# Kernel optimization log

Measured on AMD Instinct MI355X. Metric: run time of the kernel, lower is better.

The kernel has to match this reference:

```python
import jax, jax.numpy as jnp
import numpy as np

N = 100000
E = 3200000
D = 128
EPS = 1e-5


def setup_inputs() -> dict:
    key = jax.random.key(0)
    ks = jax.random.split(key, 9)
    h = jax.random.normal(ks[0], (N, D), dtype=jnp.float32)
    src = jax.random.randint(ks[1], (E,), 0, N, dtype=jnp.int64)
    dst = jax.random.randint(ks[2], (E,), 0, N, dtype=jnp.int64)
    s = 1.0 / np.sqrt(D)
    W_self = jax.random.uniform(ks[3], (D, D), jnp.float32, -s, s)
    W_neigh = jax.random.uniform(ks[4], (D, D), jnp.float32, -s, s)
    b = jax.random.uniform(ks[5], (D,), jnp.float32, -s, s)
    gamma = jnp.ones((D,), jnp.float32)
    beta = jnp.zeros((D,), jnp.float32)
    return {"h": h, "src": src, "dst": dst, "W_self": W_self,
            "W_neigh": W_neigh, "b": b, "gamma": gamma, "beta": beta}


def reference(h, src, dst, W_self, W_neigh, b, gamma, beta):
    # --- SAGEConv, mean aggregator (dropout p=0 -> identity) ---
    # gather source features along edges, segment-mean into destination nodes
    neigh_sum = jax.ops.segment_sum(h[src], dst, num_segments=N)      # [N, D]
    deg = jax.ops.segment_sum(jnp.ones((E,), h.dtype), dst, num_segments=N)
    neigh = neigh_sum / jnp.maximum(deg, 1.0)[:, None]                # [N, D]
    rst = h @ W_self + neigh @ W_neigh + b                            # [N, D]
    rst = jax.nn.relu(rst)                                            # activation
    # --- BatchNorm1d (training-mode batch statistics) ---
    mean = jnp.mean(rst, axis=0)
    var = jnp.var(rst, axis=0)
    rst = (rst - mean) * jax.lax.rsqrt(var + EPS) * gamma + beta
    # --- residual (in_feats == out_feats) ---
    return h + rst
```

## Files before the change

kernel.cpp:

```cpp
#include <hip/hip_runtime.h>

#define DCAP 2432
#define NBMAX 1600
#define SCATB 256
#define SORTCAP 12544
#define CONVB 2048
#define WPB 128
#define ZB 7
#define GB 1024
#define EORDCAP 3456

typedef __attribute__((ext_vector_type(2))) float f32x2;
typedef __attribute__((ext_vector_type(4))) float f32x4;
typedef __attribute__((ext_vector_type(8))) short bf16x8;

__device__ __forceinline__ unsigned short f2bf(float f) {
  union { float f; unsigned u; } c; c.f = f;
  unsigned u = c.u;
  unsigned r = u + 0x7FFFu + ((u >> 16) & 1u);
  return (unsigned short)(r >> 16);
}
__device__ __forceinline__ float bf2f(unsigned short s) {
  union { unsigned u; float f; } c; c.u = ((unsigned)s) << 16;
  return c.f;
}

__global__ __launch_bounds__(256) void k_pre(const float* __restrict__ h,
                                             unsigned short* __restrict__ X,
                                             unsigned* __restrict__ X8,
                                             const float* __restrict__ Ws,
                                             const float* __restrict__ Wn,
                                             unsigned short* __restrict__ Wt,
                                             int* __restrict__ gcur,
                                             int nnodes, int NB) {
  int t = threadIdx.x;
  int bid = blockIdx.x;
  if (bid < CONVB) {
    int stride = CONVB * 256;
    int total = nnodes * 32;
    for (int i = bid * 256 + t; i < total; i += stride) {
      int n = i >> 5, c = i & 31;
      float4 v = *(const float4*)(h + (long)n * 128 + c * 4);
      ushort4 o;
      o.x = f2bf(v.x); o.y = f2bf(v.y); o.z = f2bf(v.z); o.w = f2bf(v.w);
      *(ushort4*)(X + (long)n * 256 + c * 4) = o;
      int p8 = __builtin_amdgcn_cvt_pk_fp8_f32(v.x, v.y, 0, false);
      p8 = __builtin_amdgcn_cvt_pk_fp8_f32(v.z, v.w, p8, true);
      X8[(long)n * 32 + c] = (unsigned)p8;
    }
  } else if (bid < CONVB + WPB) {
    int i = (bid - CONVB) * 256 + t;
    int col = i >> 8, k = i & 255;
    float v = (k < 128) ? Ws[k * 128 + col] : Wn[(k - 128) * 128 + col];
    Wt[col * 256 + k] = f2bf(v);
  } else {
    int i = (bid - CONVB - WPB) * 256 + t;
    if (i < NB) gcur[i] = 0;
    if (i < 32) X8[(long)nnodes * 32 + i] = 0u;
  }
}

__global__ __launch_bounds__(1024) void k_scat(const int* __restrict__ dst,
                                               const int* __restrict__ src,
                                               unsigned* __restrict__ esort,
                                               int* __restrict__ gcur,
                                               int E, int NB, int chunk) {
  __shared__ int cnt[NBMAX];
  __shared__ int lstart[NBMAX];
  __shared__ int gbase[NBMAX];
  __shared__ int tsum[1024];
  __shared__ unsigned sorted[SORTCAP];
  __shared__ unsigned short sbk[SORTCAP];
  int t = threadIdx.x, bid = blockIdx.x;
  int e0 = bid * chunk;
  int e1 = e0 + chunk; if (e1 > E) e1 = E;
  int n = e1 - e0;
  for (int i = t; i < NB; i += 1024) cnt[i] = 0;
  __syncthreads();
  for (int i = t; i < n; i += 1024)
    atomicAdd(&cnt[dst[e0 + i] >> 6], 1);
  __syncthreads();
  int b0 = 2 * t, b1 = 2 * t + 1;
  int c0 = (b0 < NB) ? cnt[b0] : 0;
  int c1 = (b1 < NB) ? cnt[b1] : 0;
  tsum[t] = c0 + c1;
  __syncthreads();
  for (int off = 1; off < 1024; off <<= 1) {
    int v = (t >= off) ? tsum[t - off] : 0;
    __syncthreads();
    tsum[t] += v;
    __syncthreads();
  }
  int ex = tsum[t] - (c0 + c1);
  if (b0 < NB) {
    lstart[b0] = ex;
    cnt[b0] = ex;
    if (b1 < NB) { lstart[b1] = ex + c0; cnt[b1] = ex + c0; }
  }
  __syncthreads();
  for (int i = t; i < n; i += 1024) {
    int d = dst[e0 + i];
    int bb = d >> 6;
    int p = atomicAdd(&cnt[bb], 1);
    sorted[p] = ((unsigned)src[e0 + i] << 6) | (unsigned)(d & 63);
    sbk[p] = (unsigned short)bb;
  }
  __syncthreads();
  for (int bb = t; bb < NB; bb += 1024) {
    int len = cnt[bb] - lstart[bb];
    gbase[bb] = len ? atomicAdd(&gcur[bb], len) : 0;
  }
  __syncthreads();
  for (int i = t; i < n; i += 1024) {
    int bb = sbk[i];
    int pos = gbase[bb] + (i - lstart[bb]);
    if (pos < DCAP)
      esort[(long)bb * DCAP + pos] = sorted[i];
  }
}

__global__ __launch_bounds__(256) void k_aggb(unsigned short* __restrict__ X,
                                              const unsigned char* __restrict__ X8,
                                              const unsigned* __restrict__ esort,
                                              const int* __restrict__ gcur,
                                              int nnodes) {
  __shared__ unsigned eord[EORDCAP];
  __shared__ int dcnt[64], dstart[64], dcur[64], sc[64];
  int t = threadIdx.x;
  int b = blockIdx.x;
  int cntE = gcur[b]; if (cntE > DCAP) cntE = DCAP;
  const unsigned* ep = esort + (long)b * DCAP;
  if (t < 64) dcnt[t] = 0;
  __syncthreads();
  for (int i = t; i < cntE; i += 256)
    atomicAdd(&dcnt[ep[i] & 63u], 1);
  __syncthreads();
  int plen_t = 0;
  if (t < 64) { plen_t = (dcnt[t] + 15) & ~15; sc[t] = plen_t; }
  __syncthreads();
  for (int off = 1; off < 64; off <<= 1) {
    int v = (t < 64 && t >= off) ? sc[t - off] : 0;
    __syncthreads();
    if (t < 64) sc[t] += v;
    __syncthreads();
  }
  if (t < 64) { int ex = sc[t] - plen_t; dstart[t] = ex; dcur[t] = ex; }
  __syncthreads();
  int tot = sc[63];
  for (int i = t; i < tot; i += 256) eord[i] = (unsigned)nnodes;
  __syncthreads();
  for (int i = t; i < cntE; i += 256) {
    unsigned e = ep[i];
    int pos = atomicAdd(&dcur[e & 63u], 1);
    eord[pos] = e >> 6;
  }
  __syncthreads();

  int lane = t & 63, w = t >> 6;
  int qt = lane >> 4, ql = lane & 15;
  int ndst = nnodes - b * 64; if (ndst > 64) ndst = 64;
  for (int dl = w; dl < ndst; dl += 4) {
    int start = dstart[dl], dn = dcnt[dl];
    int plen = (dn + 15) & ~15;
    f32x2 acc[2][4];
#pragma unroll
    for (int u = 0; u < 2; u++)
#pragma unroll
      for (int j = 0; j < 4; j++) { acc[u][j].x = 0.f; acc[u][j].y = 0.f; }
    int i = 0;
    for (; i + 32 <= plen; i += 32) {
      uint2 v[8];
#pragma unroll
      for (int u = 0; u < 8; u++) {
        unsigned e = eord[start + i + u * 4 + qt];
        v[u] = *(const uint2*)(X8 + e * 128u + ql * 8u);
      }
#pragma unroll
      for (int u = 0; u < 8; u++) {
        acc[u & 1][0] += __builtin_amdgcn_cvt_pk_f32_fp8(v[u].x, false);
        acc[u & 1][1] += __builtin_amdgcn_cvt_pk_f32_fp8(v[u].x, true);
        acc[u & 1][2] += __builtin_amdgcn_cvt_pk_f32_fp8(v[u].y, false);
        acc[u & 1][3] += __builtin_amdgcn_cvt_pk_f32_fp8(v[u].y, true);
      }
    }
    if (i < plen) {
      uint2 v[4];
#pragma unroll
      for (int u = 0; u < 4; u++) {
        unsigned e = eord[start + i + u * 4 + qt];
        v[u] = *(const uint2*)(X8 + e * 128u + ql * 8u);
      }
#pragma unroll
      for (int u = 0; u < 4; u++) {
        acc[u & 1][0] += __builtin_amdgcn_cvt_pk_f32_fp8(v[u].x, false);
        acc[u & 1][1] += __builtin_amdgcn_cvt_pk_f32_fp8(v[u].x, true);
        acc[u & 1][2] += __builtin_amdgcn_cvt_pk_f32_fp8(v[u].y, false);
        acc[u & 1][3] += __builtin_amdgcn_cvt_pk_f32_fp8(v[u].y, true);
      }
    }
    float s[8];
#pragma unroll
    for (int j = 0; j < 4; j++) {
      s[2 * j] = acc[0][j].x + acc[1][j].x;
      s[2 * j + 1] = acc[0][j].y + acc[1][j].y;
    }
#pragma unroll
    for (int j = 0; j < 8; j++) {
      s[j] += __shfl_down(s[j], 32);
      s[j] += __shfl_down(s[j], 16);
    }
    if (qt == 0) {
      float scl = 1.0f / fmaxf((float)dn, 1.0f);
      uint4 o;
      o.x = (unsigned)f2bf(s[0] * scl) | ((unsigned)f2bf(s[1] * scl) << 16);
      o.y = (unsigned)f2bf(s[2] * scl) | ((unsigned)f2bf(s[3] * scl) << 16);
      o.z = (unsigned)f2bf(s[4] * scl) | ((unsigned)f2bf(s[5] * scl) << 16);
      o.w = (unsigned)f2bf(s[6] * scl) | ((unsigned)f2bf(s[7] * scl) << 16);
      *(uint4*)(X + (long)(b * 64 + dl) * 256 + 128 + ql * 8) = o;
    }
  }
}

__global__ __launch_bounds__(256) void k_gemm(const unsigned short* __restrict__ X,
                                              const unsigned short* __restrict__ Wt,
                                              const float* __restrict__ bias,
                                              unsigned short* __restrict__ rst8,
                                              float* __restrict__ psum,
                                              float* __restrict__ psq,
                                              int nnodes, int ntiles) {
  int t = threadIdx.x;
  int w = t >> 6, lane = t & 63;
  int m = lane & 15, q = lane >> 4;
  int col0 = w * 32 + m;
  int col1 = col0 + 16;
  bf16x8 b0[8], b1[8];
#pragma unroll
  for (int ks = 0; ks < 8; ks++) {
    b0[ks] = *(const bf16x8*)(Wt + col0 * 256 + q * 8 + ks * 32);
    b1[ks] = *(const bf16x8*)(Wt + col1 * 256 + q * 8 + ks * 32);
  }
  float bv0 = bias[col0], bv1 = bias[col1];
  float s0 = 0.f, sq0 = 0.f, s1 = 0.f, sq1 = 0.f;

  for (int tb = blockIdx.x; tb < ntiles; tb += GB) {
    int rowm = tb * 16 + m; if (rowm >= nnodes) rowm = nnodes - 1;
    const unsigned short* xp = X + (long)rowm * 256 + q * 8;
    bf16x8 a[8];
#pragma unroll
    for (int ks = 0; ks < 8; ks++) a[ks] = *(const bf16x8*)(xp + ks * 32);
    f32x4 acc0 = {0.f, 0.f, 0.f, 0.f};
    f32x4 acc1 = {0.f, 0.f, 0.f, 0.f};
#pragma unroll
    for (int ks = 0; ks < 8; ks++) {
      acc0 = __builtin_amdgcn_mfma_f32_16x16x32_bf16(a[ks], b0[ks], acc0, 0, 0, 0);
      acc1 = __builtin_amdgcn_mfma_f32_16x16x32_bf16(a[ks], b1[ks], acc1, 0, 0, 0);
    }
#pragma unroll
    for (int r = 0; r < 4; r++) {
      int row = tb * 16 + q * 4 + r;
      if (row < nnodes) {
        float v0 = acc0[r] + bv0; v0 = v0 > 0.f ? v0 : 0.f;
        float v1 = acc1[r] + bv1; v1 = v1 > 0.f ? v1 : 0.f;
        rst8[(long)row * 128 + col0] = f2bf(v0);
        rst8[(long)row * 128 + col1] = f2bf(v1);
        s0 += v0; sq0 += v0 * v0;
        s1 += v1; sq1 += v1 * v1;
      }
    }
  }
  s0 += __shfl_down(s0, 32);  s0 += __shfl_down(s0, 16);
  sq0 += __shfl_down(sq0, 32); sq0 += __shfl_down(sq0, 16);
  s1 += __shfl_down(s1, 32);  s1 += __shfl_down(s1, 16);
  sq1 += __shfl_down(sq1, 32); sq1 += __shfl_down(sq1, 16);
  if (lane < 16) {
    long o = (long)blockIdx.x * 128;
    psum[o + col0] = s0;  psum[o + col1] = s1;
    psq[o + col0] = sq0;  psq[o + col1] = sq1;
  }
}

__global__ __launch_bounds__(1024) void k_redstat(const float* __restrict__ psum,
                                                  const float* __restrict__ psq,
                                                  const float* __restrict__ gamma,
                                                  const float* __restrict__ beta,
                                                  float* __restrict__ scale,
                                                  float* __restrict__ shift, float Nf) {
  __shared__ float l1[1024], l2[1024];
  int t = threadIdx.x;
  int col = t & 127, sl = t >> 7;
  float s = 0.f, s2 = 0.f;
  for (int b = sl; b < GB; b += 8) {
    s += psum[b * 128 + col];
    s2 += psq[b * 128 + col];
  }
  l1[t] = s; l2[t] = s2;
  __syncthreads();
  if (t < 128) {
#pragma unroll
    for (int i = 1; i < 8; i++) { s += l1[t + i * 128]; s2 += l2[t + i * 128]; }
    float mean = s / Nf;
    float var = s2 / Nf - mean * mean;
    float inv = rsqrtf(var + 1e-5f);
    float scv = gamma[t] * inv;
    scale[t] = scv;
    shift[t] = beta[t] - mean * scv;
  }
}

__global__ void k_final(const float* __restrict__ h, float* __restrict__ out,
                        const unsigned short* __restrict__ rst8,
                        const float* __restrict__ scale, const float* __restrict__ shift,
                        int nnodes) {
  __shared__ float sc_s[128], sh_s[128];
  int t = threadIdx.x;
  if (t < 128) { sc_s[t] = scale[t]; sh_s[t] = shift[t]; }
  __syncthreads();
  int stride = gridDim.x * blockDim.x;
  int total = nnodes * 16;
  for (int i = blockIdx.x * blockDim.x + threadIdx.x; i < total; i += stride) {
    int c = i & 15;
    uint4 rv = *(const uint4*)(rst8 + (long)i * 8);
    float4 h0 = *(const float4*)(h + (long)i * 8);
    float4 h1 = *(const float4*)(h + (long)i * 8 + 4);
    float4 sc0 = *(const float4*)(sc_s + c * 8);
    float4 sc1 = *(const float4*)(sc_s + c * 8 + 4);
    float4 sh0 = *(const float4*)(sh_s + c * 8);
    float4 sh1 = *(const float4*)(sh_s + c * 8 + 4);
    float4 o0, o1;
    o0.x = h0.x + bf2f((unsigned short)(rv.x & 0xFFFFu)) * sc0.x + sh0.x;
    o0.y = h0.y + bf2f((unsigned short)(rv.x >> 16)) * sc0.y + sh0.y;
    o0.z = h0.z + bf2f((unsigned short)(rv.y & 0xFFFFu)) * sc0.z + sh0.z;
    o0.w = h0.w + bf2f((unsigned short)(rv.y >> 16)) * sc0.w + sh0.w;
    o1.x = h1.x + bf2f((unsigned short)(rv.z & 0xFFFFu)) * sc1.x + sh1.x;
    o1.y = h1.y + bf2f((unsigned short)(rv.z >> 16)) * sc1.y + sh1.y;
    o1.z = h1.z + bf2f((unsigned short)(rv.w & 0xFFFFu)) * sc1.z + sh1.z;
    o1.w = h1.w + bf2f((unsigned short)(rv.w >> 16)) * sc1.w + sh1.w;
    *(float4*)(out + (long)i * 8) = o0;
    *(float4*)(out + (long)i * 8 + 4) = o1;
  }
}

extern "C" void kernel_launch(void* const* d_in, const int* in_sizes, int n_in,
                              void* d_out, int out_size, void* d_ws, size_t ws_size,
                              hipStream_t stream) {
  const float* h     = (const float*)d_in[0];
  const int*   src   = (const int*)d_in[1];
  const int*   dst   = (const int*)d_in[2];
  const float* Ws    = (const float*)d_in[3];
  const float* Wn    = (const float*)d_in[4];
  const float* bias  = (const float*)d_in[5];
  const float* gamma = (const float*)d_in[6];
  const float* beta  = (const float*)d_in[7];
  float* out = (float*)d_out;

  int nnodes = in_sizes[0] / 128;
  int E = in_sizes[1];
  int NB = (nnodes + 63) >> 6;
  int ntiles = (nnodes + 15) >> 4;
  int chunk = (E + SCATB - 1) / SCATB;

  char* ws = (char*)d_ws;
  size_t off = 0;
  unsigned short* X = (unsigned short*)(ws + off); off += (size_t)nnodes * 256 * 2;
  size_t off_alias = off;
  unsigned* X8 = (unsigned*)(ws + off);            off += (size_t)(nnodes + 1) * 128;
  unsigned* esort = (unsigned*)(ws + off);         off += (size_t)NB * DCAP * 4;
  unsigned short* rst8 = (unsigned short*)(ws + off_alias);
  unsigned short* Wt = (unsigned short*)(ws + off); off += 128 * 256 * 2;
  float* psum = (float*)(ws + off);                off += (size_t)GB * 128 * 4;
  float* psq = (float*)(ws + off);                 off += (size_t)GB * 128 * 4;
  float* scale = (float*)(ws + off);               off += 512;
  float* shift = (float*)(ws + off);               off += 512;
  int* gcur = (int*)(ws + off);                    off += (size_t)NB * 4;

  k_pre<<<CONVB + WPB + ZB, 256, 0, stream>>>(h, X, X8, Ws, Wn, Wt, gcur, nnodes, NB);
  k_scat<<<SCATB, 1024, 0, stream>>>(dst, src, esort, gcur, E, NB, chunk);
  k_aggb<<<NB, 256, 0, stream>>>(X, (const unsigned char*)X8, esort, gcur, nnodes);
  k_gemm<<<GB, 256, 0, stream>>>(X, Wt, bias, rst8, psum, psq, nnodes, ntiles);
  k_redstat<<<1, 1024, 0, stream>>>(psum, psq, gamma, beta, scale, shift, (float)nnodes);
  k_final<<<4096, 256, 0, stream>>>(h, out, rst8, scale, shift, nnodes);
}
```

Measured before the change: 303.6 us.

## Fuse preprocessing with edge bucketing, double-buffer GEMM loads, parallelize stat reduction

Merges the feature conversion, weight transpose and edge-scatter kernels into one launch. The scatter drops its local prefix-sum and shared-memory staging and writes edges straight to global buckets through per-bucket atomic offsets. The GEMM now prefetches the next tile's A operands while computing the current one, and the BN statistic reduction is spread over 16 blocks instead of one. The bucket counter is zeroed with a memset, which adds a launch, and scatter writes become less coalesced because edges are no longer locally sorted before the store.

```diff
diff --git a/kernel.cpp b/kernel.cpp
--- a/kernel.cpp
+++ b/kernel.cpp
@@ -3,10 +3,8 @@
 #define DCAP 2432
 #define NBMAX 1600
 #define SCATB 256
-#define SORTCAP 12544
-#define CONVB 2048
-#define WPB 128
-#define ZB 7
+#define CONV2 512
+#define WPB2 32
 #define GB 1024
 #define EORDCAP 3456
 
@@ -25,20 +23,47 @@
   return c.f;
 }
 
-__global__ __launch_bounds__(256) void k_pre(const float* __restrict__ h,
-                                             unsigned short* __restrict__ X,
-                                             unsigned* __restrict__ X8,
-                                             const float* __restrict__ Ws,
-                                             const float* __restrict__ Wn,
-                                             unsigned short* __restrict__ Wt,
-                                             int* __restrict__ gcur,
-                                             int nnodes, int NB) {
+__global__ __launch_bounds__(1024) void k_prescat(const float* __restrict__ h,
+                                                  unsigned short* __restrict__ X,
+                                                  unsigned* __restrict__ X8,
+                                                  const float* __restrict__ Ws,
+                                                  const float* __restrict__ Wn,
+                                                  unsigned short* __restrict__ Wt,
+                                                  const int* __restrict__ dst,
+                                                  const int* __restrict__ src,
+                                                  unsigned* __restrict__ esort,
+                                                  int* __restrict__ gcur,
+                                                  int nnodes, int E, int NB, int chunk) {
+  __shared__ int cnt[NBMAX];
+  __shared__ int gbase[NBMAX];
   int t = threadIdx.x;
   int bid = blockIdx.x;
-  if (bid < CONVB) {
-    int stride = CONVB * 256;
+  if (bid < SCATB) {
+    int e0 = bid * chunk;
+    int e1 = e0 + chunk; if (e1 > E) e1 = E;
+    int n = e1 - e0;
+    for (int i = t; i < NB; i += 1024) cnt[i] = 0;
+    __syncthreads();
+    for (int i = t; i < n; i += 1024)
+      atomicAdd(&cnt[dst[e0 + i] >> 6], 1);
+    __syncthreads();
+    for (int bb = t; bb < NB; bb += 1024) {
+      int len = cnt[bb];
+      gbase[bb] = len ? atomicAdd(&gcur[bb], len) : 0;
+      cnt[bb] = 0;
+    }
+    __syncthreads();
+    for (int i = t; i < n; i += 1024) {
+      int d = dst[e0 + i];
+      int bb = d >> 6;
+      int pos = gbase[bb] + atomicAdd(&cnt[bb], 1);
+      if (pos < DCAP)
+        esort[(long)bb * DCAP + pos] = ((unsigned)src[e0 + i] << 6) | (unsigned)(d & 63);
+    }
+  } else if (bid < SCATB + CONV2) {
+    int stride = CONV2 * 1024;
     int total = nnodes * 32;
-    for (int i = bid * 256 + t; i < total; i += stride) {
+    for (int i = (bid - SCATB) * 1024 + t; i < total; i += stride) {
       int n = i >> 5, c = i & 31;
       float4 v = *(const float4*)(h + (long)n * 128 + c * 4);
       ushort4 o;
@@ -48,74 +73,13 @@
       p8 = __builtin_amdgcn_cvt_pk_fp8_f32(v.z, v.w, p8, true);
       X8[(long)n * 32 + c] = (unsigned)p8;
     }
-  } else if (bid < CONVB + WPB) {
-    int i = (bid - CONVB) * 256 + t;
+  } else if (bid < SCATB + CONV2 + WPB2) {
+    int i = (bid - SCATB - CONV2) * 1024 + t;
     int col = i >> 8, k = i & 255;
     float v = (k < 128) ? Ws[k * 128 + col] : Wn[(k - 128) * 128 + col];
     Wt[col * 256 + k] = f2bf(v);
   } else {
-    int i = (bid - CONVB - WPB) * 256 + t;
-    if (i < NB) gcur[i] = 0;
-    if (i < 32) X8[(long)nnodes * 32 + i] = 0u;
-  }
-}
-
-__global__ __launch_bounds__(1024) void k_scat(const int* __restrict__ dst,
-                                               const int* __restrict__ src,
-                                               unsigned* __restrict__ esort,
-                                               int* __restrict__ gcur,
-                                               int E, int NB, int chunk) {
-  __shared__ int cnt[NBMAX];
-  __shared__ int lstart[NBMAX];
-  __shared__ int gbase[NBMAX];
-  __shared__ int tsum[1024];
-  __shared__ unsigned sorted[SORTCAP];
-  __shared__ unsigned short sbk[SORTCAP];
-  int t = threadIdx.x, bid = blockIdx.x;
-  int e0 = bid * chunk;
-  int e1 = e0 + chunk; if (e1 > E) e1 = E;
-  int n = e1 - e0;
-  for (int i = t; i < NB; i += 1024) cnt[i] = 0;
-  __syncthreads();
-  for (int i = t; i < n; i += 1024)
-    atomicAdd(&cnt[dst[e0 + i] >> 6], 1);
-  __syncthreads();
-  int b0 = 2 * t, b1 = 2 * t + 1;
-  int c0 = (b0 < NB) ? cnt[b0] : 0;
-  int c1 = (b1 < NB) ? cnt[b1] : 0;
-  tsum[t] = c0 + c1;
-  __syncthreads();
-  for (int off = 1; off < 1024; off <<= 1) {
-    int v = (t >= off) ? tsum[t - off] : 0;
-    __syncthreads();
-    tsum[t] += v;
-    __syncthreads();
-  }
-  int ex = tsum[t] - (c0 + c1);
-  if (b0 < NB) {
-    lstart[b0] = ex;
-    cnt[b0] = ex;
-    if (b1 < NB) { lstart[b1] = ex + c0; cnt[b1] = ex + c0; }
-  }
-  __syncthreads();
-  for (int i = t; i < n; i += 1024) {
-    int d = dst[e0 + i];
-    int bb = d >> 6;
-    int p = atomicAdd(&cnt[bb], 1);
-    sorted[p] = ((unsigned)src[e0 + i] << 6) | (unsigned)(d & 63);
-    sbk[p] = (unsigned short)bb;
-  }
-  __syncthreads();
-  for (int bb = t; bb < NB; bb += 1024) {
-    int len = cnt[bb] - lstart[bb];
-    gbase[bb] = len ? atomicAdd(&gcur[bb], len) : 0;
-  }
-  __syncthreads();
-  for (int i = t; i < n; i += 1024) {
-    int bb = sbk[i];
-    int pos = gbase[bb] + (i - lstart[bb]);
-    if (pos < DCAP)
-      esort[(long)bb * DCAP + pos] = sorted[i];
+    if (t < 32) X8[(long)nnodes * 32 + t] = 0u;
   }
 }
 
@@ -242,32 +206,56 @@
   float bv0 = bias[col0], bv1 = bias[col1];
   float s0 = 0.f, sq0 = 0.f, s1 = 0.f, sq1 = 0.f;
 
-  for (int tb = blockIdx.x; tb < ntiles; tb += GB) {
-    int rowm = tb * 16 + m; if (rowm >= nnodes) rowm = nnodes - 1;
-    const unsigned short* xp = X + (long)rowm * 256 + q * 8;
-    bf16x8 a[8];
-#pragma unroll
-    for (int ks = 0; ks < 8; ks++) a[ks] = *(const bf16x8*)(xp + ks * 32);
-    f32x4 acc0 = {0.f, 0.f, 0.f, 0.f};
-    f32x4 acc1 = {0.f, 0.f, 0.f, 0.f};
-#pragma unroll
-    for (int ks = 0; ks < 8; ks++) {
-      acc0 = __builtin_amdgcn_mfma_f32_16x16x32_bf16(a[ks], b0[ks], acc0, 0, 0, 0);
-      acc1 = __builtin_amdgcn_mfma_f32_16x16x32_bf16(a[ks], b1[ks], acc1, 0, 0, 0);
-    }
-#pragma unroll
-    for (int r = 0; r < 4; r++) {
-      int row = tb * 16 + q * 4 + r;
-      if (row < nnodes) {
-        float v0 = acc0[r] + bv0; v0 = v0 > 0.f ? v0 : 0.f;
-        float v1 = acc1[r] + bv1; v1 = v1 > 0.f ? v1 : 0.f;
-        rst8[(long)row * 128 + col0] = f2bf(v0);
-        rst8[(long)row * 128 + col1] = f2bf(v1);
-        s0 += v0; sq0 += v0 * v0;
-        s1 += v1; sq1 += v1 * v1;
-      }
-    }
-  }
+#define LOADA(dst_, tb_)                                              \
+  {                                                                   \
+    int rowm_ = (tb_) * 16 + m;                                       \
+    if (rowm_ >= nnodes) rowm_ = nnodes - 1;                          \
+    const unsigned short* xp_ = X + (long)rowm_ * 256 + q * 8;        \
+    _Pragma("unroll")                                                 \
+    for (int ks = 0; ks < 8; ks++) dst_[ks] = *(const bf16x8*)(xp_ + ks * 32); \
+  }
+
+#define COMPUTE(a_, tb_)                                              \
+  {                                                                   \
+    f32x4 acc0 = {0.f, 0.f, 0.f, 0.f};                                \
+    f32x4 acc1 = {0.f, 0.f, 0.f, 0.f};                                \
+    _Pragma("unroll")                                                 \
+    for (int ks = 0; ks < 8; ks++) {                                  \
+      acc0 = __builtin_amdgcn_mfma_f32_16x16x32_bf16(a_[ks], b0[ks], acc0, 0, 0, 0); \
+      acc1 = __builtin_amdgcn_mfma_f32_16x16x32_bf16(a_[ks], b1[ks], acc1, 0, 0, 0); \
+    }                                                                 \
+    _Pragma("unroll")                                                 \
+    for (int r = 0; r < 4; r++) {                                     \
+      int row = (tb_) * 16 + q * 4 + r;                               \
+      if (row < nnodes) {                                             \
+        float v0 = acc0[r] + bv0; v0 = v0 > 0.f ? v0 : 0.f;           \
+        float v1 = acc1[r] + bv1; v1 = v1 > 0.f ? v1 : 0.f;           \
+        rst8[(long)row * 128 + col0] = f2bf(v0);                      \
+        rst8[(long)row * 128 + col1] = f2bf(v1);                      \
+        s0 += v0; sq0 += v0 * v0;                                     \
+        s1 += v1; sq1 += v1 * v1;                                     \
+      }                                                               \
+    }                                                                 \
+  }
+
+  int tb = blockIdx.x;
+  if (tb < ntiles) {
+    bf16x8 aA[8], aB[8];
+    LOADA(aA, tb);
+    for (; tb < ntiles; tb += 2 * GB) {
+      int tb1 = tb + GB;
+      if (tb1 < ntiles) LOADA(aB, tb1);
+      COMPUTE(aA, tb);
+      if (tb1 < ntiles) {
+        int tb2 = tb1 + GB;
+        if (tb2 < ntiles) LOADA(aA, tb2);
+        COMPUTE(aB, tb1);
+      }
+    }
+  }
+#undef LOADA
+#undef COMPUTE
+
   s0 += __shfl_down(s0, 32);  s0 += __shfl_down(s0, 16);
   sq0 += __shfl_down(sq0, 32); sq0 += __shfl_down(sq0, 16);
   s1 += __shfl_down(s1, 32);  s1 += __shfl_down(s1, 16);
@@ -279,31 +267,32 @@
   }
 }
 
-__global__ __launch_bounds__(1024) void k_redstat(const float* __restrict__ psum,
-                                                  const float* __restrict__ psq,
-                                                  const float* __restrict__ gamma,
-                                                  const float* __restrict__ beta,
-                                                  float* __restrict__ scale,
-                                                  float* __restrict__ shift, float Nf) {
-  __shared__ float l1[1024], l2[1024];
-  int t = threadIdx.x;
-  int col = t & 127, sl = t >> 7;
+__global__ __launch_bounds__(256) void k_redstat(const float* __restrict__ psum,
+                                                 const float* __restrict__ psq,
+                                                 const float* __restrict__ gamma,
+                                                 const float* __restrict__ beta,
+                                                 float* __restrict__ scale,
+                                                 float* __restrict__ shift, float Nf) {
+  __shared__ float l1[256], l2[256];
+  int t = threadIdx.x;
+  int c = t & 7, sl = t >> 3;
+  int col = blockIdx.x * 8 + c;
   float s = 0.f, s2 = 0.f;
-  for (int b = sl; b < GB; b += 8) {
+  for (int b = sl; b < GB; b += 32) {
     s += psum[b * 128 + col];
     s2 += psq[b * 128 + col];
   }
   l1[t] = s; l2[t] = s2;
   __syncthreads();
-  if (t < 128) {
-#pragma unroll
-    for (int i = 1; i < 8; i++) { s += l1[t + i * 128]; s2 += l2[t + i * 128]; }
+  if (t < 8) {
+#pragma unroll
+    for (int i = 1; i < 32; i++) { s += l1[t + i * 8]; s2 += l2[t + i * 8]; }
     float mean = s / Nf;
     float var = s2 / Nf - mean * mean;
     float inv = rsqrtf(var + 1e-5f);
-    float scv = gamma[t] * inv;
-    scale[t] = scv;
-    shift[t] = beta[t] - mean * scv;
+    float scv = gamma[col] * inv;
+    scale[col] = scv;
+    shift[col] = beta[col] - mean * scv;
   }
 }
 
@@ -373,10 +362,11 @@
   float* shift = (float*)(ws + off);               off += 512;
   int* gcur = (int*)(ws + off);                    off += (size_t)NB * 4;
 
-  k_pre<<<CONVB + WPB + ZB, 256, 0, stream>>>(h, X, X8, Ws, Wn, Wt, gcur, nnodes, NB);
-  k_scat<<<SCATB, 1024, 0, stream>>>(dst, src, esort, gcur, E, NB, chunk);
+  hipMemsetAsync(gcur, 0, (size_t)NB * 4, stream);
+  k_prescat<<<SCATB + CONV2 + WPB2 + 1, 1024, 0, stream>>>(
+      h, X, X8, Ws, Wn, Wt, dst, src, esort, gcur, nnodes, E, NB, chunk);
   k_aggb<<<NB, 256, 0, stream>>>(X, (const unsigned char*)X8, esort, gcur, nnodes);
   k_gemm<<<GB, 256, 0, stream>>>(X, Wt, bias, rst8, psum, psq, nnodes, ntiles);
-  k_redstat<<<1, 1024, 0, stream>>>(psum, psq, gamma, beta, scale, shift, (float)nnodes);
+  k_redstat<<<16, 256, 0, stream>>>(psum, psq, gamma, beta, scale, shift, (float)nnodes);
   k_final<<<4096, 256, 0, stream>>>(h, out, rst8, scale, shift, nnodes);
 }
```

Measured after the change: 300.5 us. Within noise of the previous version (-1.0%).
